# Kernel optimization log

Hardware: AMD Instinct MI355X
Metric: run time of the kernel (lower is better)

## Reference

```python
import jax, jax.numpy as jnp
import numpy as np

SOS = 1  # vocab.word2idx[SYM_SOS]


def _lstm_cell(x, h, c, Wih, Whh, b):
    # PyTorch LSTMCell gate order: i, f, g, o
    g = x @ Wih.T + h @ Whh.T + b
    i, f, gg, o = jnp.split(g, 4, axis=-1)
    c2 = jax.nn.sigmoid(f) * c + jax.nn.sigmoid(i) * jnp.tanh(gg)
    h2 = jax.nn.sigmoid(o) * jnp.tanh(c2)
    return h2, c2


def _attention(q, m, Wq, Wm, b, v):
    # additive attention: q [B,Dq], m [B,N,Dm] -> context [B,Dm]
    e = jnp.tanh((q @ Wq)[:, None, :] + m @ Wm + b)      # [B,N,H]
    score = jnp.einsum('bnh,h->bn', e, v)                # [B,N]
    a = jax.nn.softmax(score, axis=-1)
    return jnp.einsum('bn,bnd->bd', a, m)


def setup_inputs() -> dict:
    key = jax.random.key(0)
    ks = iter(jax.random.split(key, 32))
    B, T, V = 128, 20, 20000
    DI, DW, H = 512, 512, 1024
    s = 0.02
    d = {}
    d['img_feats'] = jax.random.normal(next(ks), (B, 36, DI), jnp.float32)
    d['ppl_feats'] = jax.random.normal(next(ks), (B, 100, DI), jnp.float32)
    d['answer_hint'] = jax.random.normal(next(ks), (B, DW), jnp.float32)
    d['question'] = jax.random.randint(next(ks), (B, T), 0, V)
    d['emb'] = jax.random.normal(next(ks), (V, DW), jnp.float32) * s
    d['pool_Wq'] = jax.random.normal(next(ks), (DW, DW), jnp.float32) * s
    d['pool_Wm'] = jax.random.normal(next(ks), (DI, DW), jnp.float32) * s
    d['pool_b'] = jnp.zeros((DW,), jnp.float32)
    d['pool_v'] = jax.random.normal(next(ks), (DW,), jnp.float32) * s
    d['img_Wq'] = jax.random.normal(next(ks), (H, H), jnp.float32) * s
    d['img_Wm'] = jax.random.normal(next(ks), (DI, H), jnp.float32) * s
    d['img_b'] = jnp.zeros((H,), jnp.float32)
    d['img_v'] = jax.random.normal(next(ks), (H,), jnp.float32) * s
    d['ppl_Wq'] = jax.random.normal(next(ks), (H, H), jnp.float32) * s
    d['ppl_Wm'] = jax.random.normal(next(ks), (DI, H), jnp.float32) * s
    d['ppl_b'] = jnp.zeros((H,), jnp.float32)
    d['ppl_v'] = jax.random.normal(next(ks), (H,), jnp.float32) * s
    d['vis_Wih'] = jax.random.normal(next(ks), (4 * H, DI + DW), jnp.float32) * s
    d['vis_Whh'] = jax.random.normal(next(ks), (4 * H, H), jnp.float32) * s
    d['vis_b'] = jnp.zeros((4 * H,), jnp.float32)
    d['lang_Wih'] = jax.random.normal(next(ks), (4 * H, H + DI), jnp.float32) * s
    d['lang_Whh'] = jax.random.normal(next(ks), (4 * H, H), jnp.float32) * s
    d['lang_b'] = jnp.zeros((4 * H,), jnp.float32)
    d['proj_W'] = jax.random.normal(next(ks), (H, V), jnp.float32) * s
    d['proj_b'] = jnp.zeros((V,), jnp.float32)
    return d


def reference(img_feats, ppl_feats, answer_hint, question, emb,
              pool_Wq, pool_Wm, pool_b, pool_v,
              img_Wq, img_Wm, img_b, img_v,
              ppl_Wq, ppl_Wm, ppl_b, ppl_v,
              vis_Wih, vis_Whh, vis_b,
              lang_Wih, lang_Whh, lang_b,
              proj_W, proj_b):
    B, T = question.shape
    H = vis_Whh.shape[1]
    # pooled image feature from answer hint (computed once)
    img_pool = _attention(answer_hint, img_feats, pool_Wq, pool_Wm, pool_b, pool_v)
    # teacher forcing inputs: SOS then question[:, :-1]
    tokens_in = jnp.concatenate(
        [jnp.full((B, 1), SOS, question.dtype), question[:, :-1]], axis=1)

    def step(carry, tok):
        h_vis, c_vis, h_lang, c_lang = carry
        dec_emb = jax.nn.relu(emb[tok])                          # [B,DW]
        x_vis = jnp.concatenate([img_pool, dec_emb], axis=-1)
        h_vis, c_vis = _lstm_cell(x_vis, h_vis, c_vis, vis_Wih, vis_Whh, vis_b)
        image_attn = _attention(h_vis, img_feats, img_Wq, img_Wm, img_b, img_v)
        ppl_attn = _attention(h_vis, ppl_feats, ppl_Wq, ppl_Wm, ppl_b, ppl_v)
        x_lang = jnp.concatenate([image_attn + ppl_attn, h_vis], axis=-1)
        h_lang, c_lang = _lstm_cell(x_lang, h_lang, c_lang, lang_Wih, lang_Whh, lang_b)
        logp = jax.nn.log_softmax(h_lang @ proj_W + proj_b, axis=-1)
        return (h_vis, c_vis, h_lang, c_lang), (logp, jnp.argmax(logp, axis=-1))

    z = jnp.zeros((B, H), img_feats.dtype)
    _, (logps, toks) = jax.lax.scan(step, (z, z, z, z), tokens_in.T)
    return jnp.transpose(logps, (1, 0, 2)), toks.T


if __name__ == '__main__':
    out = reference(**setup_inputs())
    print(out[0].shape, out[1].shape)
```

## Files before the change

kernel.cpp:

```cpp
#include <hip/hip_runtime.h>
#include <cstddef>
#include <cstdint>

using u16 = unsigned short;
typedef float    f32x4 __attribute__((ext_vector_type(4)));
typedef _Float16 f16x8 __attribute__((ext_vector_type(8)));
typedef u16      us8   __attribute__((ext_vector_type(8)));

constexpr int B  = 128;
constexpr int T  = 20;
constexpr int V  = 20000;
constexpr int DW = 512;
constexpr int H  = 1024;
constexpr int G4 = 4096;
constexpr int NI = 36;
constexpr int NP = 100;
constexpr int SOS = 1;

__device__ __forceinline__ float sigf(float x) { return 1.0f / (1.0f + expf(-x)); }
__device__ __forceinline__ u16 f16bits(_Float16 h) { u16 u; __builtin_memcpy(&u, &h, 2); return u; }
__device__ __forceinline__ float h2f(u16 u) { _Float16 h; __builtin_memcpy(&h, &u, 2); return (float)h; }

template<bool WSIDE>
__device__ __forceinline__ void split1(float x, u16& b0, u16& b1, u16& b2) {
    _Float16 h  = (_Float16)x;
    float    hf = (float)h;
    _Float16 lo = (_Float16)((x - hf) * 64.0f);
    _Float16 hs = (_Float16)(hf * (1.0f / 64.0f));
    b0 = f16bits(h);
    if constexpr (WSIDE) { b1 = f16bits(hs); b2 = f16bits(lo); }
    else                 { b1 = f16bits(lo); b2 = f16bits(hs); }
}

template<int BM, int BN, bool HAS_ADD, bool HAS_BIAS, int NSW = 0, bool OUTF16 = false>
__global__ __launch_bounds__(256)
void gemm3(const u16* __restrict__ A, const u16* __restrict__ Bt,
           const float* __restrict__ Add, const float* __restrict__ bias,
           void* __restrict__ Cv, int N, int K3)
{
    __shared__ __align__(16) u16 As[BM * 64];
    __shared__ __align__(16) u16 Bs[BN * 64];
    constexpr int FR = BM / 32, FC = BN / 32, PA = BM / 32, PB = BN / 32;
    const int tid  = threadIdx.x;
    int bx = blockIdx.x, by = blockIdx.y;
    if constexpr (NSW > 0) {
        const int nt = (int)gridDim.x, mt = (int)gridDim.y;
        const int lin = by * nt + bx;
        const int sc0 = (lin / (NSW * mt)) * NSW;
        const int w   = (NSW < nt - sc0) ? NSW : (nt - sc0);
        const int r   = lin - sc0 * mt;
        bx = sc0 + r % w;
        by = r / w;
    }
    const int bm   = by * BM, bn = bx * BN;
    const int lane = tid & 63, wid = tid >> 6;
    const int wm   = (wid >> 1) * (BM / 2), wn = (wid & 1) * (BN / 2);
    const int srow = tid >> 3;
    const int scol = (tid & 7) * 8;

    f32x4 acc[FR][FC] = {};
    us8 ra[PA], rb[PB];

    auto ldg = [&](int k0) {
#pragma unroll
        for (int p = 0; p < PA; ++p)
            ra[p] = *(const us8*)(A + (size_t)(bm + p * 32 + srow) * K3 + k0 + scol);
#pragma unroll
        for (int p = 0; p < PB; ++p) {
            int n = bn + p * 32 + srow; if (n > N - 1) n = N - 1;
            rb[p] = *(const us8*)(Bt + (size_t)n * K3 + k0 + scol);
        }
    };
    ldg(0);

    for (int k0 = 0; k0 < K3; k0 += 64) {
        __syncthreads();
#pragma unroll
        for (int p = 0; p < PA; ++p) {
            const int row = p * 32 + srow;
            *(us8*)((char*)As + row * 128 + ((scol * 2) ^ ((row & 7) << 4))) = ra[p];
        }
#pragma unroll
        for (int p = 0; p < PB; ++p) {
            const int row = p * 32 + srow;
            *(us8*)((char*)Bs + row * 128 + ((scol * 2) ^ ((row & 7) << 4))) = rb[p];
        }
        __syncthreads();
        if (k0 + 64 < K3) ldg(k0 + 64);
#pragma unroll
        for (int ks = 0; ks < 2; ++ks) {
            f16x8 af[FR], bf[FC];
#pragma unroll
            for (int m = 0; m < FR; ++m) {
                const int row = wm + m * 16 + (lane & 15);
                const int cb  = (ks * 64 + ((lane >> 4) << 4)) ^ ((row & 7) << 4);
                af[m] = *(const f16x8*)((const char*)As + row * 128 + cb);
            }
#pragma unroll
            for (int n = 0; n < FC; ++n) {
                const int row = wn + n * 16 + (lane & 15);
                const int cb  = (ks * 64 + ((lane >> 4) << 4)) ^ ((row & 7) << 4);
                bf[n] = *(const f16x8*)((const char*)Bs + row * 128 + cb);
            }
#pragma unroll
            for (int m = 0; m < FR; ++m)
#pragma unroll
                for (int n = 0; n < FC; ++n)
                    acc[m][n] = __builtin_amdgcn_mfma_f32_16x16x32_f16(af[m], bf[n], acc[m][n], 0, 0, 0);
        }
    }
#pragma unroll
    for (int m = 0; m < FR; ++m) {
        const int r0 = bm + wm + m * 16 + ((lane >> 4) << 2);
#pragma unroll
        for (int n = 0; n < FC; ++n) {
            const int c = bn + wn + n * 16 + (lane & 15);
            if (c < N) {
#pragma unroll
                for (int j = 0; j < 4; ++j) {
                    float v = acc[m][n][j];
                    if constexpr (HAS_ADD)  v += Add[(size_t)(r0 + j) * N + c];
                    if constexpr (HAS_BIAS) v += bias[c];
                    if constexpr (OUTF16)
                        ((u16*)Cv)[(size_t)(r0 + j) * N + c] = f16bits((_Float16)v);
                    else
                        ((float*)Cv)[(size_t)(r0 + j) * N + c] = v;
                }
            }
        }
    }
}

template<int EPI, int BN, int BK>
__device__ __forceinline__ void gemm_core(
    u16* As, u16* Bs,
    const u16* A, const u16* Bt,
    const float* Add, const float* bias,
    float* CS, u16* o1, u16* o2,
    int N, int K3, int t, int bx, int by)
{
    constexpr int NA8  = BK / 32;
    constexpr int TPRB = 256 / BN;
    constexpr int NB8  = (BK / TPRB) / 8;
    constexpr int NFC  = BN / 16;
    const int tid  = threadIdx.x;
    const int bn   = bx * BN, bm = by * 64;
    const int lane = tid & 63, wv = tid >> 6;
    const int rowA = tid >> 2;
    const int scA  = (tid & 3) * (BK / 4);
    const int rowB = tid / TPRB;
    const int scB  = (tid % TPRB) * (BK / TPRB);
    const int swzA = (rowA & 7) << 4;
    const int swzB = (rowB & 7) << 4;
    const u16* Ap = A  + (size_t)(bm + rowA) * K3 + scA;
    const u16* Bp = Bt + (size_t)(bn + rowB) * K3 + scB;
    char* Awp = (char*)As + rowA * (BK * 2);
    char* Bwp = (char*)Bs + rowB * (BK * 2);
    const int arow = wv * 16 + (lane & 15);
    const char* Arp = (const char*)As + arow * (BK * 2);
    const int aswz = (arow & 7) << 4;
    const int jl   = lane & 15;

    f32x4 acc[NFC] = {};
    us8 ra[NA8], rb[NB8];
#pragma unroll
    for (int i = 0; i < NA8; ++i) ra[i] = *(const us8*)(Ap + 8 * i);
#pragma unroll
    for (int i = 0; i < NB8; ++i) rb[i] = *(const us8*)(Bp + 8 * i);

    for (int k0 = 0; k0 < K3; k0 += BK) {
        __syncthreads();
#pragma unroll
        for (int i = 0; i < NA8; ++i)
            *(us8*)(Awp + ((scA * 2 + 16 * i) ^ swzA)) = ra[i];
#pragma unroll
        for (int i = 0; i < NB8; ++i)
            *(us8*)(Bwp + ((scB * 2 + 16 * i) ^ swzB)) = rb[i];
        __syncthreads();
        if (k0 + BK < K3) {
#pragma unroll
            for (int i = 0; i < NA8; ++i) ra[i] = *(const us8*)(Ap + k0 + BK + 8 * i);
#pragma unroll
            for (int i = 0; i < NB8; ++i) rb[i] = *(const us8*)(Bp + k0 + BK + 8 * i);
        }
#pragma unroll
        for (int ks = 0; ks < BK / 32; ++ks) {
            const int cb = ks * 64 + ((lane >> 4) << 4);
            const f16x8 af = *(const f16x8*)(Arp + (cb ^ aswz));
#pragma unroll
            for (int g = 0; g < NFC; ++g) {
                const int brow = g * 16 + jl;
                const f16x8 bf = *(const f16x8*)((const char*)Bs + brow * (BK * 2) + (cb ^ ((brow & 7) << 4)));
                acc[g] = __builtin_amdgcn_mfma_f32_16x16x32_f16(af, bf, acc[g], 0, 0, 0);
            }
        }
    }
    const int rb0 = bm + wv * 16 + ((lane >> 4) << 2);
    if constexpr (EPI == 0) {
#pragma unroll
        for (int g = 0; g < NFC; ++g) {
            const int c = bn + g * 16 + jl;
#pragma unroll
            for (int jj = 0; jj < 4; ++jj)
                CS[(size_t)(rb0 + jj) * N + c] = acc[g][jj];
        }
    } else {
        const int j = bx * 16 + jl;
#pragma unroll
        for (int jj = 0; jj < 4; ++jj) {
            const int b = rb0 + jj;
            float gi = acc[0][jj], gf = acc[1][jj], gg = acc[2][jj], go = acc[3][jj];
            if constexpr (EPI == 1) {
                const float* ap = Add + (size_t)b * 4096 + bn + jl;
                gi += ap[0]; gf += ap[16]; gg += ap[32]; go += ap[48];
            } else {
                const float* bp = bias + bn + jl;
                gi += bp[0]; gf += bp[16]; gg += bp[32]; go += bp[48];
            }
            const float c = sigf(gf) * CS[b * 1024 + j] + sigf(gi) * tanhf(gg);
            const float h = sigf(go) * tanhf(c);
            CS[b * 1024 + j] = c;
            u16 b0, b1, b2; split1<false>(h, b0, b1, b2);
            if constexpr (EPI == 1) {
                u16* a = o1 + (size_t)b * 3072 + j;
                a[0] = b0; a[1024] = b1; a[2048] = b2;
                u16* x = o2 + (size_t)b * 7680 + 512 + j;
                x[0] = b0; x[2560] = b1; x[5120] = b2;
            } else {
                u16* x = o1 + (size_t)b * 7680 + 1536 + j;
                x[0] = b0; x[2560] = b1; x[5120] = b2;
                u16* hh = o2 + ((size_t)b * T + t) * 3072 + j;
                hh[0] = b0; hh[1024] = b1; hh[2048] = b2;
            }
        }
    }
}

__global__ __launch_bounds__(256)
void gemm_q(const u16* __restrict__ A, const u16* __restrict__ Bt,
            float* __restrict__ CS, int N, int K3)
{
    __shared__ __align__(16) u16 As[64 * 384];
    __shared__ __align__(16) u16 Bs[16 * 384];
    gemm_core<0, 16, 384>(As, Bs, A, Bt, nullptr, nullptr, CS, nullptr, nullptr,
                          N, K3, 0, blockIdx.x, blockIdx.y);
}

__global__ __launch_bounds__(256)
void step_combo(const u16* __restrict__ lang_A, const u16* __restrict__ langW3,
                const float* __restrict__ lang_bi, float* c_lang,
                u16* lang_o1, u16* h3_all,
                const u16* __restrict__ vis_A, const u16* __restrict__ visWhh3,
                const float* __restrict__ g_pre_t, float* c_vis,
                u16* vis_o1, u16* vis_o2, int t)
{
    __shared__ __align__(16) u16 As[64 * 384];
    __shared__ __align__(16) u16 Bs[64 * 384];
    if (blockIdx.z == 0) {
        if (t >= 1)
            gemm_core<2, 64, 384>(As, Bs, lang_A, langW3, nullptr, lang_bi,
                                  c_lang, lang_o1, h3_all, G4, 7680, t - 1,
                                  blockIdx.x, blockIdx.y);
    } else {
        if (t < T)
            gemm_core<1, 64, 384>(As, Bs, vis_A, visWhh3, g_pre_t, nullptr,
                                  c_vis, vis_o1, vis_o2, G4, 3072, t,
                                  blockIdx.x, blockIdx.y);
    }
}

template<bool WSIDE>
__global__ __launch_bounds__(256)
void split3_rows(const float* __restrict__ src, int ld, int K8,
                 u16* __restrict__ out, int Kt, int coloff)
{
    const int idx = blockIdx.x * 256 + threadIdx.x;
    const int r = idx / K8, kk = (idx - r * K8) * 8;
    const float* s = src + (size_t)r * ld + kk;
    const float4 x0 = *(const float4*)s, x1 = *(const float4*)(s + 4);
    float xs[8] = {x0.x, x0.y, x0.z, x0.w, x1.x, x1.y, x1.z, x1.w};
    us8 h, m, l;
#pragma unroll
    for (int j = 0; j < 8; ++j) { u16 a, b, c; split1<WSIDE>(xs[j], a, b, c); h[j]=a; m[j]=b; l[j]=c; }
    u16* o = out + (size_t)r * (3 * Kt) + coloff + kk;
    *(us8*)o = h; *(us8*)(o + Kt) = m; *(us8*)(o + 2 * Kt) = l;
}

__global__ __launch_bounds__(256)
void split3_lstm(const float* __restrict__ src, int ld, int K8,
                 u16* __restrict__ out, int Kt, int coloff)
{
    const int idx = blockIdx.x * 256 + threadIdx.x;
    const int r = idx / K8, kk = (idx - r * K8) * 8;
    const int g = r >> 10, j = r & 1023;
    const int orow = ((j >> 4) << 6) + (g << 4) + (j & 15);
    const float* s = src + (size_t)r * ld + kk;
    const float4 x0 = *(const float4*)s, x1 = *(const float4*)(s + 4);
    float xs[8] = {x0.x, x0.y, x0.z, x0.w, x1.x, x1.y, x1.z, x1.w};
    us8 h, m, l;
#pragma unroll
    for (int jj = 0; jj < 8; ++jj) { u16 a, b, c; split1<true>(xs[jj], a, b, c); h[jj]=a; m[jj]=b; l[jj]=c; }
    u16* o = out + (size_t)orow * (3 * Kt) + coloff + kk;
    *(us8*)o = h; *(us8*)(o + Kt) = m; *(us8*)(o + 2 * Kt) = l;
}

__global__ __launch_bounds__(256)
void permute_bias_lstm(const float* __restrict__ b, float* __restrict__ out)
{
    const int c = blockIdx.x * 256 + threadIdx.x;
    const int jg = c >> 6, g = (c >> 4) & 3, jlo = c & 15;
    out[c] = b[g * 1024 + jg * 16 + jlo];
}

__global__ __launch_bounds__(256)
void transpose_split3_w(const float* __restrict__ W, int N, int K,
                        u16* __restrict__ out)
{
    const int n0 = blockIdx.x * 64, k0 = blockIdx.y * 64;
    const int tid = threadIdx.x;
    __shared__ float ts[64][65];
    for (int i = 0; i < 16; ++i) {
        const int idx = i * 256 + tid;
        const int kl = idx >> 6, nl = idx & 63;
        float v = 0.f;
        if (n0 + nl < N) v = W[(size_t)(k0 + kl) * N + n0 + nl];
        ts[nl][kl] = v;
    }
    __syncthreads();
    for (int i = 0; i < 2; ++i) {
        const int idx = i * 256 + tid;
        const int nl = idx >> 3, kc = (idx & 7) * 8;
        if (n0 + nl < N) {
            us8 h, m, l;
#pragma unroll
            for (int j = 0; j < 8; ++j) {
                u16 a, b, c; split1<true>(ts[nl][kc + j], a, b, c);
                h[j] = a; m[j] = b; l[j] = c;
            }
            u16* o = out + (size_t)(n0 + nl) * (3 * K) + k0 + kc;
            *(us8*)o = h; *(us8*)(o + K) = m; *(us8*)(o + 2 * K) = l;
        }
    }
}

__global__ __launch_bounds__(256)
void embed_relu3(const int* __restrict__ question, const float* __restrict__ emb,
                 u16* __restrict__ A2)
{
    const int idx = blockIdx.x * 256 + threadIdx.x;
    const int r = idx >> 6, kk = (idx & 63) * 8;
    const int t = r / B, b = r - t * B;
    const int tok = (t == 0) ? SOS : question[b * T + t - 1];
    const float* s = emb + (size_t)tok * DW + kk;
    const float4 x0 = *(const float4*)s, x1 = *(const float4*)(s + 4);
    float xs[8] = {x0.x, x0.y, x0.z, x0.w, x1.x, x1.y, x1.z, x1.w};
    us8 h, m, l;
#pragma unroll
    for (int j = 0; j < 8; ++j) {
        u16 a, b2, c; split1<false>(fmaxf(xs[j], 0.f), a, b2, c);
        h[j] = a; m[j] = b2; l[j] = c;
    }
    u16* o = A2 + (size_t)r * 3072 + 512 + kk;
    *(us8*)o = h; *(us8*)(o + 1024) = m; *(us8*)(o + 2048) = l;
}

__global__ __launch_bounds__(256)
void attn_score(const float* __restrict__ q, int qld,
                const float* __restrict__ mW, const float* __restrict__ v,
                float* __restrict__ score, int Nn, int Hd)
{
    const int n = blockIdx.x, b = blockIdx.y;
    const float* qp = q + (size_t)b * qld;
    const float* mp = mW + ((size_t)b * Nn + n) * Hd;
    float s = 0.f;
    for (int h = threadIdx.x; h < Hd; h += 256)
        s += tanhf(qp[h] + mp[h]) * v[h];
    __shared__ float red[4];
    const int lane = threadIdx.x & 63, wv = threadIdx.x >> 6;
    for (int o = 32; o; o >>= 1) s += __shfl_down(s, o, 64);
    if (lane == 0) red[wv] = s;
    __syncthreads();
    if (threadIdx.x == 0) score[(size_t)b * Nn + n] = red[0] + red[1] + red[2] + red[3];
}

__global__ __launch_bounds__(256)
void attn_ctx_pool(const float* __restrict__ score, const float* __restrict__ m,
                   u16* __restrict__ A2, int Nn)
{
    constexpr int D = 512;
    const int b = blockIdx.x;
    __shared__ float aw[128];
    __shared__ float red[8];
    const int tid = threadIdx.x, lane = tid & 63, wv = tid >> 6;
    float mx = -3.4e38f;
    for (int n = tid; n < Nn; n += 256) mx = fmaxf(mx, score[(size_t)b * Nn + n]);
    for (int o = 32; o; o >>= 1) mx = fmaxf(mx, __shfl_down(mx, o, 64));
    if (lane == 0) red[wv] = mx;
    __syncthreads();
    mx = fmaxf(fmaxf(red[0], red[1]), fmaxf(red[2], red[3]));
    float se = 0.f;
    for (int n = tid; n < Nn; n += 256) {
        float e = expf(score[(size_t)b * Nn + n] - mx);
        aw[n] = e; se += e;
    }
    for (int o = 32; o; o >>= 1) se += __shfl_down(se, o, 64);
    if (lane == 0) red[4 + wv] = se;
    __syncthreads();
    const float inv = 1.0f / (red[4] + red[5] + red[6] + red[7]);
    for (int d = tid; d < D; d += 256) {
        float s = 0.f;
        for (int n = 0; n < Nn; ++n) s += aw[n] * m[((size_t)b * Nn + n) * D + d];
        s *= inv;
        u16 b0, b1, b2; split1<false>(s, b0, b1, b2);
        for (int tt = 0; tt < T; ++tt) {
            u16* o = A2 + ((size_t)tt * B + b) * 3072 + d;
            o[0] = b0; o[1024] = b1; o[2048] = b2;
        }
    }
}

__global__ __launch_bounds__(512)
void attn_fused(const float* __restrict__ qbuf,
                const u16* __restrict__ img_mW, const u16* __restrict__ ppl_mW,
                const float* __restrict__ img_v, const float* __restrict__ ppl_v,
                const float* __restrict__ img_feats, const float* __restrict__ ppl_feats,
                u16* __restrict__ x3)
{
    const int b = blockIdx.x;
    const int tid = threadIdx.x, lane = tid & 63, wv = tid >> 6;
    __shared__ float qs[2048];
    __shared__ float vs[2048];
    __shared__ float aw[136];
    __shared__ float awn[136];

    for (int i = tid; i < 2048; i += 512) {
        qs[i] = qbuf[(size_t)b * 2048 + i];
        vs[i] = (i < 1024) ? img_v[i] : ppl_v[i - 1024];
    }
    __syncthreads();

    for (int n = wv; n < NI; n += 8) {
        const u16* mp = img_mW + ((size_t)b * NI + n) * 1024;
        float s = 0.f;
#pragma unroll
        for (int u = 0; u < 2; ++u) {
            const int h = (lane + 64 * u) * 8;
            const us8 m8 = *(const us8*)(mp + h);
#pragma unroll
            for (int j = 0; j < 8; ++j)
                s += tanhf(qs[h + j] + h2f(m8[j])) * vs[h + j];
        }
        for (int o = 1; o < 64; o <<= 1) s += __shfl_xor(s, o, 64);
        if (lane == 0) aw[n] = s;
    }
    for (int n = wv; n < NP; n += 8) {
        const u16* mp = ppl_mW + ((size_t)b * NP + n) * 1024;
        float s = 0.f;
#pragma unroll
        for (int u = 0; u < 2; ++u) {
            const int h = (lane + 64 * u) * 8;
            const us8 m8 = *(const us8*)(mp + h);
#pragma unroll
            for (int j = 0; j < 8; ++j)
                s += tanhf(qs[1024 + h + j] + h2f(m8[j])) * vs[1024 + h + j];
        }
        for (int o = 1; o < 64; o <<= 1) s += __shfl_xor(s, o, 64);
        if (lane == 0) aw[36 + n] = s;
    }
    __syncthreads();

    if (wv == 0) {
        const float x = (lane < NI) ? aw[lane] : -3.4e38f;
        float mx = x;
        for (int o = 1; o < 64; o <<= 1) mx = fmaxf(mx, __shfl_xor(mx, o, 64));
        const float e = (lane < NI) ? expf(x - mx) : 0.f;
        float ss = e;
        for (int o = 1; o < 64; o <<= 1) ss += __shfl_xor(ss, o, 64);
        if (lane < NI) awn[lane] = e / ss;
    } else if (wv == 1) {
        const float x0 = aw[36 + lane];
        const float x1 = (lane < NP - 64) ? aw[100 + lane] : -3.4e38f;
        float mx = fmaxf(x0, x1);
        for (int o = 1; o < 64; o <<= 1) mx = fmaxf(mx, __shfl_xor(mx, o, 64));
        const float e0 = expf(x0 - mx);
        const float e1 = (lane < NP - 64) ? expf(x1 - mx) : 0.f;
        float ss = e0 + e1;
        for (int o = 1; o < 64; o <<= 1) ss += __shfl_xor(ss, o, 64);
        awn[36 + lane] = e0 / ss;
        if (lane < NP - 64) awn[100 + lane] = e1 / ss;
    }
    __syncthreads();

    {
        const int d = tid;
        float s = 0.f;
        const float* ip = img_feats + (size_t)b * NI * 512 + d;
#pragma unroll 4
        for (int n = 0; n < NI; ++n) s += awn[n] * ip[n * 512];
        const float* pp = ppl_feats + (size_t)b * NP * 512 + d;
#pragma unroll 4
        for (int n = 0; n < NP; ++n) s += awn[36 + n] * pp[n * 512];
        u16 b0, b1, b2; split1<false>(s, b0, b1, b2);
        u16* o = x3 + (size_t)b * 7680 + d;
        o[0] = b0; o[2560] = b1; o[5120] = b2;
    }
}

__global__ __launch_bounds__(256)
void zero_f(float* __restrict__ p) { p[blockIdx.x * 256 + threadIdx.x] = 0.f; }

__global__ __launch_bounds__(256)
void zero_u32(unsigned int* __restrict__ p) { p[blockIdx.x * 256 + threadIdx.x] = 0u; }

__global__ __launch_bounds__(256)
void logsm_argmax(float* __restrict__ out)
{
    const int r = blockIdx.x;
    float* row = out + (size_t)r * V;
    const int tid = threadIdx.x, lane = tid & 63, wv = tid >> 6;
    float m = -3.4e38f, s = 0.f; int mi = 0;
    for (int i4 = tid; i4 < V / 4; i4 += 256) {
        const float4 x4 = ((const float4*)row)[i4];
        const float xs[4] = {x4.x, x4.y, x4.z, x4.w};
#pragma unroll
        for (int j = 0; j < 4; ++j) {
            const float x = xs[j];
            if (x > m) { s = s * expf(m - x) + 1.f; m = x; mi = i4 * 4 + j; }
            else       s += expf(x - m);
        }
    }
    for (int o = 1; o < 64; o <<= 1) {
        const float m2 = __shfl_xor(m, o, 64);
        const float s2 = __shfl_xor(s, o, 64);
        const int  mi2 = __shfl_xor(mi, o, 64);
        if (m2 > m || (m2 == m && mi2 < mi)) { s = s2 + s * expf(m - m2); m = m2; mi = mi2; }
        else s += s2 * expf(m2 - m);
    }
    __shared__ float sm[4], ssm[4]; __shared__ int smi[4];
    __shared__ float lse_sh; __shared__ int mi_sh;
    if (lane == 0) { sm[wv] = m; ssm[wv] = s; smi[wv] = mi; }
    __syncthreads();
    if (tid == 0) {
        float M = sm[0], S = ssm[0]; int MI = smi[0];
        for (int w = 1; w < 4; ++w) {
            if (sm[w] > M || (sm[w] == M && smi[w] < MI)) { S = ssm[w] + S * expf(M - sm[w]); M = sm[w]; MI = smi[w]; }
            else S += ssm[w] * expf(sm[w] - M);
        }
        lse_sh = M + logf(S); mi_sh = MI;
    }
    __syncthreads();
    const float lse = lse_sh;
    for (int i4 = tid; i4 < V / 4; i4 += 256) {
        float4 x4 = ((const float4*)row)[i4];
        x4.x -= lse; x4.y -= lse; x4.z -= lse; x4.w -= lse;
        ((float4*)row)[i4] = x4;
    }
    if (tid == 0) out[(size_t)B * T * V + r] = (float)mi_sh;
}

extern "C" void kernel_launch(void* const* d_in, const int* in_sizes, int n_in,
                              void* d_out, int out_size, void* d_ws, size_t ws_size,
                              hipStream_t stream)
{
    (void)in_sizes; (void)n_in; (void)out_size; (void)ws_size;

    const float* img_feats   = (const float*)d_in[0];
    const float* ppl_feats   = (const float*)d_in[1];
    const float* answer_hint = (const float*)d_in[2];
    const int*   question    = (const int*)d_in[3];
    const float* emb         = (const float*)d_in[4];
    const float* pool_Wq     = (const float*)d_in[5];
    const float* pool_Wm     = (const float*)d_in[6];
    const float* pool_b      = (const float*)d_in[7];
    const float* pool_v      = (const float*)d_in[8];
    const float* img_Wq      = (const float*)d_in[9];
    const float* img_Wm      = (const float*)d_in[10];
    const float* img_b       = (const float*)d_in[11];
    const float* img_v       = (const float*)d_in[12];
    const float* ppl_Wq      = (const float*)d_in[13];
    const float* ppl_Wm      = (const float*)d_in[14];
    const float* ppl_b       = (const float*)d_in[15];
    const float* ppl_v       = (const float*)d_in[16];
    const float* vis_Wih     = (const float*)d_in[17];
    const float* vis_Whh     = (const float*)d_in[18];
    const float* vis_b       = (const float*)d_in[19];
    const float* lang_Wih    = (const float*)d_in[20];
    const float* lang_Whh    = (const float*)d_in[21];
    const float* lang_b      = (const float*)d_in[22];
    const float* proj_W      = (const float*)d_in[23];
    const float* proj_b      = (const float*)d_in[24];

    float* out = (float*)d_out;
    float* ws  = (float*)d_ws;

    size_t off = 0;
    auto alloc = [&](size_t nf) { size_t r = off; off += (nf + 63) & ~(size_t)63; return r; };
    const size_t regionX = off;
    float* g_pre   = ws + alloc((size_t)T * B * G4);
    float* pool_mW = ws + alloc((size_t)B * NI * DW);
    u16*   A2      = (u16*)(ws + alloc((size_t)T * B * 3072 / 2));
    u16*   hint3   = (u16*)(ws + alloc((size_t)B * 1536 / 2));
    u16*   poolWq3t= (u16*)(ws + alloc((size_t)512 * 1536 / 2));
    u16*   poolWm3t= (u16*)(ws + alloc((size_t)512 * 1536 / 2));
    u16*   visWih3 = (u16*)(ws + alloc((size_t)G4 * 3072 / 2));
    u16*   img_mW  = (u16*)(ws + alloc((size_t)B * NI * H / 2));
    u16*   ppl_mW  = (u16*)(ws + alloc((size_t)B * NP * H / 2));
    u16*   img3    = (u16*)(ws + alloc((size_t)B * NI * 1536 / 2));
    u16*   ppl3    = (u16*)(ws + alloc((size_t)B * NP * 1536 / 2));
    u16* visWhh3   = (u16*)(ws + alloc((size_t)G4 * 3072 / 2));
    u16* langW3    = (u16*)(ws + alloc((size_t)G4 * 7680 / 2));
    u16* wq3t      = (u16*)(ws + alloc((size_t)2048 * 3072 / 2));
    u16* imgWm3t   = (u16*)(ws + alloc((size_t)1024 * 1536 / 2));
    u16* pplWm3t   = (u16*)(ws + alloc((size_t)1024 * 1536 / 2));
    float* c_vis   = ws + alloc((size_t)B * H);
    float* c_lang  = ws + alloc((size_t)B * H);
    u16* a3        = (u16*)(ws + alloc((size_t)2 * B * 3072 / 2));
    u16* x3        = (u16*)(ws + alloc((size_t)2 * B * 7680 / 2));
    u16* h3_all    = (u16*)(ws + alloc((size_t)B * T * 3072 / 2));
    float* qbuf    = ws + alloc((size_t)B * 2048);
    float* vis_bi  = ws + alloc((size_t)G4);
    float* lang_bi = ws + alloc((size_t)G4);
    float* pool_qW = ws + alloc((size_t)B * DW);
    float* pool_sc = ws + alloc((size_t)B * NI);
    u16* projW3t   = (u16*)(ws + regionX);

    const dim3 blk(256);

    zero_f<<<dim3((2 * B * H) / 256), blk, 0, stream>>>(c_vis);
    zero_u32<<<dim3((2 * B * 3072 + 2 * B * 7680) / 2 / 256), blk, 0, stream>>>((unsigned int*)a3);

    embed_relu3<<<dim3(T * B * 64 / 256), blk, 0, stream>>>(question, emb, A2);
    permute_bias_lstm<<<dim3(16), blk, 0, stream>>>(vis_b, vis_bi);
    permute_bias_lstm<<<dim3(16), blk, 0, stream>>>(lang_b, lang_bi);
    split3_lstm<<<dim3(G4 * 128 / 256), blk, 0, stream>>>(vis_Wih, 1024, 128, visWih3, 1024, 0);
    split3_lstm<<<dim3(G4 * 128 / 256), blk, 0, stream>>>(vis_Whh, 1024, 128, visWhh3, 1024, 0);
    split3_lstm<<<dim3(G4 * 192 / 256), blk, 0, stream>>>(lang_Wih, 1536, 192, langW3, 2560, 0);
    split3_lstm<<<dim3(G4 * 128 / 256), blk, 0, stream>>>(lang_Whh, 1024, 128, langW3, 2560, 1536);
    split3_rows<false><<<dim3(B * NI * 64 / 256), blk, 0, stream>>>(img_feats, 512, 64, img3, 512, 0);
    split3_rows<false><<<dim3(B * NP * 64 / 256), blk, 0, stream>>>(ppl_feats, 512, 64, ppl3, 512, 0);
    split3_rows<false><<<dim3(B * 64 / 256), blk, 0, stream>>>(answer_hint, 512, 64, hint3, 512, 0);
    transpose_split3_w<<<dim3(8, 8), blk, 0, stream>>>(pool_Wq, 512, 512, poolWq3t);
    transpose_split3_w<<<dim3(8, 8), blk, 0, stream>>>(pool_Wm, 512, 512, poolWm3t);
    transpose_split3_w<<<dim3(16, 8), blk, 0, stream>>>(img_Wm, 1024, 512, imgWm3t);
    transpose_split3_w<<<dim3(16, 8), blk, 0, stream>>>(ppl_Wm, 1024, 512, pplWm3t);
    transpose_split3_w<<<dim3(16, 16), blk, 0, stream>>>(img_Wq, 1024, 1024, wq3t);
    transpose_split3_w<<<dim3(16, 16), blk, 0, stream>>>(ppl_Wq, 1024, 1024, wq3t + (size_t)1024 * 3072);

    gemm3<64, 64, false, false><<<dim3(8, 2), blk, 0, stream>>>(hint3, poolWq3t, nullptr, nullptr, pool_qW, 512, 1536);
    gemm3<128, 128, false, true><<<dim3(4, 36), blk, 0, stream>>>(img3, poolWm3t, nullptr, pool_b, pool_mW, 512, 1536);
    attn_score<<<dim3(NI, B), blk, 0, stream>>>(pool_qW, 512, pool_mW, pool_v, pool_sc, NI, 512);
    attn_ctx_pool<<<dim3(B), blk, 0, stream>>>(pool_sc, img_feats, A2, NI);
    gemm3<128, 128, false, true><<<dim3(32, 20), blk, 0, stream>>>(A2, visWih3, nullptr, vis_bi, g_pre, G4, 3072);
    gemm3<128, 128, false, true, 0, true><<<dim3(8, 36), blk, 0, stream>>>(img3, imgWm3t, nullptr, img_b, img_mW, H, 1536);
    gemm3<128, 128, false, true, 0, true><<<dim3(8, 100), blk, 0, stream>>>(ppl3, pplWm3t, nullptr, ppl_b, ppl_mW, H, 1536);

    for (int t = 0; t <= T; ++t) {
        u16* lang_A  = x3 + (size_t)((t + 1) & 1) * B * 7680;
        u16* lang_o1 = x3 + (size_t)(t & 1) * B * 7680;
        u16* vis_A   = a3 + (size_t)(t & 1) * B * 3072;
        u16* vis_o1  = a3 + (size_t)((t + 1) & 1) * B * 3072;
        u16* vis_o2  = x3 + (size_t)(t & 1) * B * 7680;
        const float* gp = g_pre + (size_t)(t < T ? t : 0) * B * G4;
        step_combo<<<dim3(64, 2, 2), blk, 0, stream>>>(
            lang_A, langW3, lang_bi, c_lang, lang_o1, h3_all,
            vis_A, visWhh3, gp, c_vis, vis_o1, vis_o2, t);
        if (t < T) {
            gemm_q<<<dim3(128, 2), blk, 0, stream>>>(vis_o1, wq3t, qbuf, 2048, 3072);
            attn_fused<<<dim3(B), dim3(512), 0, stream>>>(qbuf, img_mW, ppl_mW, img_v, ppl_v,
                                                          img_feats, ppl_feats, vis_o2);
        }
    }

    transpose_split3_w<<<dim3(313, 16), blk, 0, stream>>>(proj_W, V, 1024, projW3t);
    gemm3<128, 128, false, true, 20><<<dim3(157, 20), blk, 0, stream>>>(
        h3_all, projW3t, nullptr, proj_b, out, V, 3072);
    logsm_argmax<<<dim3(B * T), blk, 0, stream>>>(out);
}
```

Before: 3.579 ms.

## Split lang LSTM recurrent GEMM off the critical path and overlap with query GEMM

The language LSTM's h_lang @ Whh product is separated from the input-side GEMM and computed in a new combined kernel alongside the attention query projection. Its bias-added gates go to a buffer, and the step kernel then adds them in the epilogue. This shortens the K dimension of the lang-LSTM GEMM on the serial critical path, from 7680 to 4608, and uses otherwise idle blocks during the query GEMM. It adds a gates buffer round-trip, changes the buffer layouts, and also changes a template parameter of the final projection GEMM.

```diff
diff --git a/kernel.cpp b/kernel.cpp
--- a/kernel.cpp
+++ b/kernel.cpp
@@ -196,13 +196,16 @@
         }
     }
     const int rb0 = bm + wv * 16 + ((lane >> 4) << 2);
-    if constexpr (EPI == 0) {
+    if constexpr (EPI == 0 || EPI == 3) {
 #pragma unroll
         for (int g = 0; g < NFC; ++g) {
             const int c = bn + g * 16 + jl;
 #pragma unroll
-            for (int jj = 0; jj < 4; ++jj)
-                CS[(size_t)(rb0 + jj) * N + c] = acc[g][jj];
+            for (int jj = 0; jj < 4; ++jj) {
+                float v = acc[g][jj];
+                if constexpr (EPI == 3) v += bias[c];
+                CS[(size_t)(rb0 + jj) * N + c] = v;
+            }
         }
     } else {
         const int j = bx * 16 + jl;
@@ -210,12 +213,9 @@
         for (int jj = 0; jj < 4; ++jj) {
             const int b = rb0 + jj;
             float gi = acc[0][jj], gf = acc[1][jj], gg = acc[2][jj], go = acc[3][jj];
-            if constexpr (EPI == 1) {
+            {
                 const float* ap = Add + (size_t)b * 4096 + bn + jl;
                 gi += ap[0]; gf += ap[16]; gg += ap[32]; go += ap[48];
-            } else {
-                const float* bp = bias + bn + jl;
-                gi += bp[0]; gf += bp[16]; gg += bp[32]; go += bp[48];
             }
             const float c = sigf(gf) * CS[b * 1024 + j] + sigf(gi) * tanhf(gg);
             const float h = sigf(go) * tanhf(c);
@@ -224,11 +224,11 @@
             if constexpr (EPI == 1) {
                 u16* a = o1 + (size_t)b * 3072 + j;
                 a[0] = b0; a[1024] = b1; a[2048] = b2;
-                u16* x = o2 + (size_t)b * 7680 + 512 + j;
-                x[0] = b0; x[2560] = b1; x[5120] = b2;
+                u16* x = o2 + (size_t)b * 4608 + 512 + j;
+                x[0] = b0; x[1536] = b1; x[3072] = b2;
             } else {
-                u16* x = o1 + (size_t)b * 7680 + 1536 + j;
-                x[0] = b0; x[2560] = b1; x[5120] = b2;
+                u16* hl = o1 + (size_t)b * 3072 + j;
+                hl[0] = b0; hl[1024] = b1; hl[2048] = b2;
                 u16* hh = o2 + ((size_t)b * T + t) * 3072 + j;
                 hh[0] = b0; hh[1024] = b1; hh[2048] = b2;
             }
@@ -237,19 +237,30 @@
 }
 
 __global__ __launch_bounds__(256)
-void gemm_q(const u16* __restrict__ A, const u16* __restrict__ Bt,
-            float* __restrict__ CS, int N, int K3)
+void gemm_q_hh(const u16* __restrict__ a3_new, const u16* __restrict__ wq3t,
+               float* qbuf,
+               const u16* __restrict__ hl_prev, const u16* __restrict__ langWhh3,
+               const float* __restrict__ lang_bi, float* gates_hh)
 {
     __shared__ __align__(16) u16 As[64 * 384];
-    __shared__ __align__(16) u16 Bs[16 * 384];
-    gemm_core<0, 16, 384>(As, Bs, A, Bt, nullptr, nullptr, CS, nullptr, nullptr,
-                          N, K3, 0, blockIdx.x, blockIdx.y);
-}
-
-__global__ __launch_bounds__(256)
-void step_combo(const u16* __restrict__ lang_A, const u16* __restrict__ langW3,
-                const float* __restrict__ lang_bi, float* c_lang,
-                u16* lang_o1, u16* h3_all,
+    __shared__ __align__(16) u16 Bs[32 * 384];
+    const int blk = blockIdx.x;
+    if (blk < 256) {
+        gemm_core<0, 16, 384>(As, Bs, a3_new, wq3t, nullptr, nullptr,
+                              qbuf, nullptr, nullptr, 2048, 3072, 0,
+                              blk & 127, blk >> 7);
+    } else {
+        const int b2 = blk - 256;
+        gemm_core<3, 32, 384>(As, Bs, hl_prev, langWhh3, nullptr, lang_bi,
+                              gates_hh, nullptr, nullptr, 4096, 3072, 0,
+                              b2 & 127, b2 >> 7);
+    }
+}
+
+__global__ __launch_bounds__(256)
+void step_combo(const u16* __restrict__ lang_A, const u16* __restrict__ langWih3,
+                const float* __restrict__ gates_hh, float* c_lang,
+                u16* hl_out, u16* h3_all,
                 const u16* __restrict__ vis_A, const u16* __restrict__ visWhh3,
                 const float* __restrict__ g_pre_t, float* c_vis,
                 u16* vis_o1, u16* vis_o2, int t)
@@ -258,8 +269,8 @@
     __shared__ __align__(16) u16 Bs[64 * 384];
     if (blockIdx.z == 0) {
         if (t >= 1)
-            gemm_core<2, 64, 384>(As, Bs, lang_A, langW3, nullptr, lang_bi,
-                                  c_lang, lang_o1, h3_all, G4, 7680, t - 1,
+            gemm_core<2, 64, 384>(As, Bs, lang_A, langWih3, gates_hh, nullptr,
+                                  c_lang, hl_out, h3_all, G4, 4608, t - 1,
                                   blockIdx.x, blockIdx.y);
     } else {
         if (t < T)
@@ -424,7 +435,7 @@
                 const u16* __restrict__ img_mW, const u16* __restrict__ ppl_mW,
                 const float* __restrict__ img_v, const float* __restrict__ ppl_v,
                 const float* __restrict__ img_feats, const float* __restrict__ ppl_feats,
-                u16* __restrict__ x3)
+                u16* __restrict__ x4)
 {
     const int b = blockIdx.x;
     const int tid = threadIdx.x, lane = tid & 63, wv = tid >> 6;
@@ -501,8 +512,8 @@
 #pragma unroll 4
         for (int n = 0; n < NP; ++n) s += awn[36 + n] * pp[n * 512];
         u16 b0, b1, b2; split1<false>(s, b0, b1, b2);
-        u16* o = x3 + (size_t)b * 7680 + d;
-        o[0] = b0; o[2560] = b1; o[5120] = b2;
+        u16* o = x4 + (size_t)b * 4608 + d;
+        o[0] = b0; o[1536] = b1; o[3072] = b2;
     }
 }
 
@@ -608,16 +619,19 @@
     u16*   img3    = (u16*)(ws + alloc((size_t)B * NI * 1536 / 2));
     u16*   ppl3    = (u16*)(ws + alloc((size_t)B * NP * 1536 / 2));
     u16* visWhh3   = (u16*)(ws + alloc((size_t)G4 * 3072 / 2));
-    u16* langW3    = (u16*)(ws + alloc((size_t)G4 * 7680 / 2));
+    u16* langWih3  = (u16*)(ws + alloc((size_t)G4 * 4608 / 2));
+    u16* langWhh3  = (u16*)(ws + alloc((size_t)G4 * 3072 / 2));
     u16* wq3t      = (u16*)(ws + alloc((size_t)2048 * 3072 / 2));
     u16* imgWm3t   = (u16*)(ws + alloc((size_t)1024 * 1536 / 2));
     u16* pplWm3t   = (u16*)(ws + alloc((size_t)1024 * 1536 / 2));
     float* c_vis   = ws + alloc((size_t)B * H);
     float* c_lang  = ws + alloc((size_t)B * H);
     u16* a3        = (u16*)(ws + alloc((size_t)2 * B * 3072 / 2));
-    u16* x3        = (u16*)(ws + alloc((size_t)2 * B * 7680 / 2));
+    u16* x4        = (u16*)(ws + alloc((size_t)2 * B * 4608 / 2));
+    u16* hl3       = (u16*)(ws + alloc((size_t)2 * B * 3072 / 2));
     u16* h3_all    = (u16*)(ws + alloc((size_t)B * T * 3072 / 2));
     float* qbuf    = ws + alloc((size_t)B * 2048);
+    float* gates_hh= ws + alloc((size_t)B * G4);
     float* vis_bi  = ws + alloc((size_t)G4);
     float* lang_bi = ws + alloc((size_t)G4);
     float* pool_qW = ws + alloc((size_t)B * DW);
@@ -627,15 +641,15 @@
     const dim3 blk(256);
 
     zero_f<<<dim3((2 * B * H) / 256), blk, 0, stream>>>(c_vis);
-    zero_u32<<<dim3((2 * B * 3072 + 2 * B * 7680) / 2 / 256), blk, 0, stream>>>((unsigned int*)a3);
+    zero_u32<<<dim3(5376), blk, 0, stream>>>((unsigned int*)a3);
 
     embed_relu3<<<dim3(T * B * 64 / 256), blk, 0, stream>>>(question, emb, A2);
     permute_bias_lstm<<<dim3(16), blk, 0, stream>>>(vis_b, vis_bi);
     permute_bias_lstm<<<dim3(16), blk, 0, stream>>>(lang_b, lang_bi);
     split3_lstm<<<dim3(G4 * 128 / 256), blk, 0, stream>>>(vis_Wih, 1024, 128, visWih3, 1024, 0);
     split3_lstm<<<dim3(G4 * 128 / 256), blk, 0, stream>>>(vis_Whh, 1024, 128, visWhh3, 1024, 0);
-    split3_lstm<<<dim3(G4 * 192 / 256), blk, 0, stream>>>(lang_Wih, 1536, 192, langW3, 2560, 0);
-    split3_lstm<<<dim3(G4 * 128 / 256), blk, 0, stream>>>(lang_Whh, 1024, 128, langW3, 2560, 1536);
+    split3_lstm<<<dim3(G4 * 192 / 256), blk, 0, stream>>>(lang_Wih, 1536, 192, langWih3, 1536, 0);
+    split3_lstm<<<dim3(G4 * 128 / 256), blk, 0, stream>>>(lang_Whh, 1024, 128, langWhh3, 1024, 0);
     split3_rows<false><<<dim3(B * NI * 64 / 256), blk, 0, stream>>>(img_feats, 512, 64, img3, 512, 0);
     split3_rows<false><<<dim3(B * NP * 64 / 256), blk, 0, stream>>>(ppl_feats, 512, 64, ppl3, 512, 0);
     split3_rows<false><<<dim3(B * 64 / 256), blk, 0, stream>>>(answer_hint, 512, 64, hint3, 512, 0);
@@ -655,24 +669,26 @@
     gemm3<128, 128, false, true, 0, true><<<dim3(8, 100), blk, 0, stream>>>(ppl3, pplWm3t, nullptr, ppl_b, ppl_mW, H, 1536);
 
     for (int t = 0; t <= T; ++t) {
-        u16* lang_A  = x3 + (size_t)((t + 1) & 1) * B * 7680;
-        u16* lang_o1 = x3 + (size_t)(t & 1) * B * 7680;
+        u16* x4_prev = x4 + (size_t)((t + 1) & 1) * B * 4608;
+        u16* x4_cur  = x4 + (size_t)(t & 1) * B * 4608;
         u16* vis_A   = a3 + (size_t)(t & 1) * B * 3072;
         u16* vis_o1  = a3 + (size_t)((t + 1) & 1) * B * 3072;
-        u16* vis_o2  = x3 + (size_t)(t & 1) * B * 7680;
+        u16* hl_prev = hl3 + (size_t)((t + 1) & 1) * B * 3072;
+        u16* hl_out  = hl_prev;
         const float* gp = g_pre + (size_t)(t < T ? t : 0) * B * G4;
         step_combo<<<dim3(64, 2, 2), blk, 0, stream>>>(
-            lang_A, langW3, lang_bi, c_lang, lang_o1, h3_all,
-            vis_A, visWhh3, gp, c_vis, vis_o1, vis_o2, t);
+            x4_prev, langWih3, gates_hh, c_lang, hl_out, h3_all,
+            vis_A, visWhh3, gp, c_vis, vis_o1, x4_cur, t);
         if (t < T) {
-            gemm_q<<<dim3(128, 2), blk, 0, stream>>>(vis_o1, wq3t, qbuf, 2048, 3072);
+            gemm_q_hh<<<dim3(512), blk, 0, stream>>>(
+                vis_o1, wq3t, qbuf, hl_prev, langWhh3, lang_bi, gates_hh);
             attn_fused<<<dim3(B), dim3(512), 0, stream>>>(qbuf, img_mW, ppl_mW, img_v, ppl_v,
-                                                          img_feats, ppl_feats, vis_o2);
+                                                          img_feats, ppl_feats, x4_cur);
         }
     }
 
     transpose_split3_w<<<dim3(313, 16), blk, 0, stream>>>(proj_W, V, 1024, projW3t);
-    gemm3<128, 128, false, true, 20><<<dim3(157, 20), blk, 0, stream>>>(
+    gemm3<128, 128, false, true, 10><<<dim3(157, 20), blk, 0, stream>>>(
         h3_all, projW3t, nullptr, proj_b, out, V, 3072);
     logsm_argmax<<<dim3(B * T), blk, 0, stream>>>(out);
 }
```

Result: faster. 3.419 ms (-4.5%).
